# Performance work log

Measured on AMD Instinct MI355X. Metric: run time of the kernel, lower is better.

The kernel has to match this reference:

```python
import jax, jax.numpy as jnp
import numpy as np
from jax import lax

H, W = 320, 320
K = 21
P = (K - 1) // 2  # 10, replicate padding
LAM = 128.0
SIGMA_SPACE = 32.0
SIGMA_LUMA = 8.0
# all (i, j) kernel positions except the center -> 440 offsets
OFFSETS = np.array([(i, j) for i in range(K) for j in range(K)
                    if not (i == P and j == P)], dtype=np.int32)  # [440, 2]


def neighbor_diffs(x):
    """Shift-and-subtract equivalent of the sparse 21x21 conv.

    x: [H, W] -> [440, H, W] where out[k] = x - shift(x, offset_k)
    (replicate padding, matching Conv2d padding_mode='replicate' with a
    +1-at-center / -1-at-(i,j) kernel).
    """
    padded = jnp.pad(x, P, mode='edge')  # [H+2P, W+2P]

    def window(off):
        return lax.dynamic_slice(padded, (off[0], off[1]), (H, W))

    shifted = jax.vmap(window)(jnp.asarray(OFFSETS))  # [440, H, W]
    return x[None, :, :] - shifted


def setup_inputs() -> dict:
    key = jax.random.key(0)
    k_ref, k_tgt, k_noise = jax.random.split(key, 3)
    # random guidance image in [0, 255] like an RGB reference
    reference = jax.random.uniform(k_ref, (H, W, 3), dtype=jnp.float32) * 255.0
    target = jax.random.uniform(k_tgt, (H, W), dtype=jnp.float32)  # target/255
    # output parameter initialized at target (plus tiny noise so the data
    # term is non-degenerate)
    output = target + 0.01 * jax.random.normal(k_noise, (H, W), dtype=jnp.float32)

    # bilateral affinity weights w_ij, exactly as in __init__
    pos_x = jnp.broadcast_to(jnp.linspace(0.0, W, W)[None, :], (H, W))
    pos_y = jnp.broadcast_to(jnp.linspace(0.0, H, H)[:, None], (H, W))
    dpx = neighbor_diffs(pos_x)
    dpy = neighbor_diffs(pos_y)
    position_ij = -(dpx ** 2 + dpy ** 2) / (2.0 * SIGMA_SPACE ** 2)
    reference_ij = 0.0
    for c in range(3):
        reference_ij = reference_ij - neighbor_diffs(reference[:, :, c]) ** 2 / (2.0 * SIGMA_LUMA ** 2)
    w_ij = jnp.exp(position_ij + reference_ij)  # [440, H, W]

    return {"output": output, "target": target, "w_ij": w_ij}


def reference(output, target, w_ij):
    d = neighbor_diffs(output)  # [440, H, W]
    smooth = jnp.mean(w_ij * d * d)
    data = jnp.mean((output - target) ** 2)
    return H * W * LAM * smooth + data
```

## Files before the change

### kernel.cpp

```cpp
#include <hip/hip_runtime.h>
#include <cstddef>

constexpr int H_ = 320;
constexpr int W_ = 320;
constexpr int HW_ = H_ * W_;
constexpr int NK = 440;
constexpr int TS = 32;
constexpr int TPR = W_ / TS;
constexpr int NTILES = TPR * TPR;
constexpr int KC = 20;
constexpr int NKC = NK / KC;
constexpr int SMOOTH_BLOCKS = NTILES * NKC;
constexpr int NPART = SMOOTH_BLOCKS + NTILES;
constexpr int HALO = 10;
constexpr int LW = TS + 2 * HALO;
constexpr int LSTRIDE = LW + 1;

typedef float f32x4 __attribute__((ext_vector_type(4)));

__device__ __forceinline__ int clampi(int v, int lo, int hi) {
    return v < lo ? lo : (v > hi ? hi : v);
}

__device__ __forceinline__ float block_reduce(float v, float* rbuf, int tid) {
    __syncthreads();
    for (int off = 32; off > 0; off >>= 1)
        v += __shfl_down(v, off, 64);
    if ((tid & 63) == 0) rbuf[tid >> 6] = v;
    __syncthreads();
    return rbuf[0] + rbuf[1] + rbuf[2] + rbuf[3];
}

__global__ __launch_bounds__(256) void bsl_main_kernel(
    const float* __restrict__ img,
    const float* __restrict__ tgt,
    const float* __restrict__ w,
    float* __restrict__ partials)
{
    __shared__ float lds[LW * LSTRIDE];
    __shared__ float rbuf[4];
    const int tid = threadIdx.x;

    const int tileId = blockIdx.x / NKC;
    const int kc     = blockIdx.x % NKC;
    const int ty = tileId / TPR, tx = tileId % TPR;
    const int y0 = ty * TS, x0 = tx * TS;

    for (int e = tid; e < LW * LW; e += 256) {
        const int ly = e / LW, lx = e - ly * LW;
        const int gy = clampi(y0 - HALO + ly, 0, H_ - 1);
        const int gx = clampi(x0 - HALO + lx, 0, W_ - 1);
        lds[ly * LSTRIDE + lx] = img[gy * W_ + gx];
    }
    __syncthreads();

    const int row = tid >> 3;
    const int c4  = (tid & 7) * 4;
    const int cbase = (HALO + row) * LSTRIDE + HALO + c4;
    const float c0 = lds[cbase + 0];
    const float c1 = lds[cbase + 1];
    const float c2 = lds[cbase + 2];
    const float c3 = lds[cbase + 3];

    float sacc = 0.f;
    const float* wp = w + (size_t)(kc * KC) * HW_ + (y0 + row) * W_ + x0 + c4;
#pragma unroll 4
    for (int kk = 0; kk < KC; ++kk) {
        const int bk  = kc * KC + kk;
        const int idx = (bk < 220) ? bk : bk + 1;
        const int q   = idx / 21;
        const int di  = q - 10;
        const int dj  = idx - q * 21 - 10;

        const f32x4 w4 = __builtin_nontemporal_load((const f32x4*)wp);
        wp += HW_;

        const int nb = cbase + di * LSTRIDE + dj;
        const float n0 = lds[nb + 0];
        const float n1 = lds[nb + 1];
        const float n2 = lds[nb + 2];
        const float n3 = lds[nb + 3];
        const float d0 = c0 - n0, d1 = c1 - n1, d2 = c2 - n2, d3 = c3 - n3;
        sacc += w4.x * d0 * d0;
        sacc += w4.y * d1 * d1;
        sacc += w4.z * d2 * d2;
        sacc += w4.w * d3 * d3;
    }

    const float ssum = block_reduce(sacc, rbuf, tid);
    if (tid == 0) partials[blockIdx.x] = ssum;

    if (kc == 0) {
        const float4 t4 = *reinterpret_cast<const float4*>(
            tgt + (y0 + row) * W_ + x0 + c4);
        const float d0 = c0 - t4.x, d1 = c1 - t4.y;
        const float d2 = c2 - t4.z, d3 = c3 - t4.w;
        const float dsum = block_reduce(d0*d0 + d1*d1 + d2*d2 + d3*d3, rbuf, tid);
        if (tid == 0) partials[SMOOTH_BLOCKS + tileId] = dsum;
    }
}

__global__ __launch_bounds__(256) void bsl_final_kernel(
    const float* __restrict__ partials, float* __restrict__ out)
{
    const int tid = threadIdx.x;
    double s = 0.0, d = 0.0;

    for (int base = 0; base < SMOOTH_BLOCKS; base += 1024) {
        const int i = base + tid * 4;
        if (i + 4 <= SMOOTH_BLOCKS) {
            const float4 v = *reinterpret_cast<const float4*>(partials + i);
            s += (double)v.x + (double)v.y + (double)v.z + (double)v.w;
        }
    }
    if (tid < NTILES / 4) {
        const float4 v = *reinterpret_cast<const float4*>(
            partials + SMOOTH_BLOCKS + tid * 4);
        d += (double)v.x + (double)v.y + (double)v.z + (double)v.w;
    }

    __shared__ double sm[256];
    __shared__ double sd[256];
    sm[tid] = s; sd[tid] = d;
    __syncthreads();
    for (int st = 128; st > 0; st >>= 1) {
        if (tid < st) { sm[tid] += sm[tid + st]; sd[tid] += sd[tid + st]; }
        __syncthreads();
    }
    if (tid == 0) {
        out[0] = (float)(128.0 * sm[0] / 440.0 + sd[0] / (double)HW_);
    }
}

extern "C" void kernel_launch(void* const* d_in, const int* in_sizes, int n_in,
                              void* d_out, int out_size, void* d_ws, size_t ws_size,
                              hipStream_t stream) {
    const float* img = (const float*)d_in[0];
    const float* tgt = (const float*)d_in[1];
    const float* wij = (const float*)d_in[2];
    float* out = (float*)d_out;
    float* partials = (float*)d_ws;

    bsl_main_kernel<<<SMOOTH_BLOCKS, 256, 0, stream>>>(img, tgt, wij, partials);
    bsl_final_kernel<<<1, 256, 0, stream>>>(partials, out);
}
```

Baseline: 36.26 us.

## Switch to full-width row strips with two rows per thread

Tiles change from 32x32 squares to full-width 8-row strips with 10 offsets per block and 320 threads. Each thread now handles 8 pixels across two rows, so every wij load covers 1280 contiguous floats per warp row and the LDS halo overhead per block shrinks. The trade-off is a larger LDS footprint per block (28x341 floats), a different block count, and a 5-wave reduction.

New measurement: 38.43 us. 6.0% more time.

```diff
diff --git a/kernel.cpp b/kernel.cpp
--- a/kernel.cpp
+++ b/kernel.cpp
@@ -5,16 +5,17 @@
 constexpr int W_ = 320;
 constexpr int HW_ = H_ * W_;
 constexpr int NK = 440;
-constexpr int TS = 32;
-constexpr int TPR = W_ / TS;
-constexpr int NTILES = TPR * TPR;
-constexpr int KC = 20;
+constexpr int TR = 8;
+constexpr int NTILES = H_ / TR;
+constexpr int KC = 10;
 constexpr int NKC = NK / KC;
 constexpr int SMOOTH_BLOCKS = NTILES * NKC;
 constexpr int NPART = SMOOTH_BLOCKS + NTILES;
 constexpr int HALO = 10;
-constexpr int LW = TS + 2 * HALO;
-constexpr int LSTRIDE = LW + 1;
+constexpr int LROWS = TR + 2 * HALO;
+constexpr int LCOLS = W_ + 2 * HALO;
+constexpr int LSTRIDE = LCOLS + 1;
+constexpr int NT_ = 320;
 
 typedef float f32x4 __attribute__((ext_vector_type(4)));
 
@@ -28,74 +29,94 @@
         v += __shfl_down(v, off, 64);
     if ((tid & 63) == 0) rbuf[tid >> 6] = v;
     __syncthreads();
-    return rbuf[0] + rbuf[1] + rbuf[2] + rbuf[3];
+    return rbuf[0] + rbuf[1] + rbuf[2] + rbuf[3] + rbuf[4];
 }
 
-__global__ __launch_bounds__(256) void bsl_main_kernel(
+__global__ __launch_bounds__(NT_, 5) void bsl_main_kernel(
     const float* __restrict__ img,
     const float* __restrict__ tgt,
     const float* __restrict__ w,
     float* __restrict__ partials)
 {
-    __shared__ float lds[LW * LSTRIDE];
-    __shared__ float rbuf[4];
+    __shared__ float lds[LROWS * LSTRIDE];
+    __shared__ float rbuf[5];
     const int tid = threadIdx.x;
 
     const int tileId = blockIdx.x / NKC;
     const int kc     = blockIdx.x % NKC;
-    const int ty = tileId / TPR, tx = tileId % TPR;
-    const int y0 = ty * TS, x0 = tx * TS;
+    const int y0 = tileId * TR;
 
-    for (int e = tid; e < LW * LW; e += 256) {
-        const int ly = e / LW, lx = e - ly * LW;
+    for (int e = tid; e < LROWS * LCOLS; e += NT_) {
+        const int ly = e / LCOLS, lx = e - ly * LCOLS;
         const int gy = clampi(y0 - HALO + ly, 0, H_ - 1);
-        const int gx = clampi(x0 - HALO + lx, 0, W_ - 1);
+        const int gx = clampi(lx - HALO, 0, W_ - 1);
         lds[ly * LSTRIDE + lx] = img[gy * W_ + gx];
     }
     __syncthreads();
 
-    const int row = tid >> 3;
-    const int c4  = (tid & 7) * 4;
-    const int cbase = (HALO + row) * LSTRIDE + HALO + c4;
-    const float c0 = lds[cbase + 0];
-    const float c1 = lds[cbase + 1];
-    const float c2 = lds[cbase + 2];
-    const float c3 = lds[cbase + 3];
+    const int px0 = 4 * tid;
+    const int r0  = px0 / W_;
+    const int cc  = px0 - r0 * W_;
+    const int cb0 = (HALO + r0) * LSTRIDE + HALO + cc;
+    const int cb1 = cb0 + 4 * LSTRIDE;
+    float ca[4], cb[4];
+#pragma unroll
+    for (int j = 0; j < 4; ++j) { ca[j] = lds[cb0 + j]; cb[j] = lds[cb1 + j]; }
 
     float sacc = 0.f;
-    const float* wp = w + (size_t)(kc * KC) * HW_ + (y0 + row) * W_ + x0 + c4;
-#pragma unroll 4
-    for (int kk = 0; kk < KC; ++kk) {
-        const int bk  = kc * KC + kk;
-        const int idx = (bk < 220) ? bk : bk + 1;
-        const int q   = idx / 21;
-        const int di  = q - 10;
-        const int dj  = idx - q * 21 - 10;
+    const float* wq = w + (size_t)(kc * KC) * HW_ + y0 * W_ + px0;
+    for (int kk = 0; kk < KC; kk += 2) {
+        const int bka  = kc * KC + kk;
+        const int idxa = (bka < 220) ? bka : bka + 1;
+        const int qa   = idxa / 21;
+        const int sofa = (qa - 10) * LSTRIDE + (idxa - qa * 21 - 10);
+        const int bkb  = bka + 1;
+        const int idxb = (bkb < 220) ? bkb : bkb + 1;
+        const int qb   = idxb / 21;
+        const int sofb = (qb - 10) * LSTRIDE + (idxb - qb * 21 - 10);
 
-        const f32x4 w4 = __builtin_nontemporal_load((const f32x4*)wp);
-        wp += HW_;
+        const f32x4 wa0 = __builtin_nontemporal_load((const f32x4*)(wq));
+        const f32x4 wa1 = __builtin_nontemporal_load((const f32x4*)(wq + 1280));
+        const f32x4 wb0 = __builtin_nontemporal_load((const f32x4*)(wq + HW_));
+        const f32x4 wb1 = __builtin_nontemporal_load((const f32x4*)(wq + HW_ + 1280));
+        wq += 2 * HW_;
 
-        const int nb = cbase + di * LSTRIDE + dj;
-        const float n0 = lds[nb + 0];
-        const float n1 = lds[nb + 1];
-        const float n2 = lds[nb + 2];
-        const float n3 = lds[nb + 3];
-        const float d0 = c0 - n0, d1 = c1 - n1, d2 = c2 - n2, d3 = c3 - n3;
-        sacc += w4.x * d0 * d0;
-        sacc += w4.y * d1 * d1;
-        sacc += w4.z * d2 * d2;
-        sacc += w4.w * d3 * d3;
+        {
+            const int n0 = cb0 + sofa, n1 = cb1 + sofa;
+            const float d0 = ca[0] - lds[n0 + 0], d1 = ca[1] - lds[n0 + 1];
+            const float d2 = ca[2] - lds[n0 + 2], d3 = ca[3] - lds[n0 + 3];
+            const float e0 = cb[0] - lds[n1 + 0], e1 = cb[1] - lds[n1 + 1];
+            const float e2 = cb[2] - lds[n1 + 2], e3 = cb[3] - lds[n1 + 3];
+            sacc += wa0.x * d0 * d0 + wa0.y * d1 * d1
+                  + wa0.z * d2 * d2 + wa0.w * d3 * d3;
+            sacc += wa1.x * e0 * e0 + wa1.y * e1 * e1
+                  + wa1.z * e2 * e2 + wa1.w * e3 * e3;
+        }
+        {
+            const int n0 = cb0 + sofb, n1 = cb1 + sofb;
+            const float d0 = ca[0] - lds[n0 + 0], d1 = ca[1] - lds[n0 + 1];
+            const float d2 = ca[2] - lds[n0 + 2], d3 = ca[3] - lds[n0 + 3];
+            const float e0 = cb[0] - lds[n1 + 0], e1 = cb[1] - lds[n1 + 1];
+            const float e2 = cb[2] - lds[n1 + 2], e3 = cb[3] - lds[n1 + 3];
+            sacc += wb0.x * d0 * d0 + wb0.y * d1 * d1
+                  + wb0.z * d2 * d2 + wb0.w * d3 * d3;
+            sacc += wb1.x * e0 * e0 + wb1.y * e1 * e1
+                  + wb1.z * e2 * e2 + wb1.w * e3 * e3;
+        }
     }
 
     const float ssum = block_reduce(sacc, rbuf, tid);
     if (tid == 0) partials[blockIdx.x] = ssum;
 
     if (kc == 0) {
-        const float4 t4 = *reinterpret_cast<const float4*>(
-            tgt + (y0 + row) * W_ + x0 + c4);
-        const float d0 = c0 - t4.x, d1 = c1 - t4.y;
-        const float d2 = c2 - t4.z, d3 = c3 - t4.w;
-        const float dsum = block_reduce(d0*d0 + d1*d1 + d2*d2 + d3*d3, rbuf, tid);
+        const float4 t0 = *reinterpret_cast<const float4*>(tgt + y0 * W_ + px0);
+        const float4 t1 = *reinterpret_cast<const float4*>(tgt + y0 * W_ + 1280 + px0);
+        const float d0 = ca[0] - t0.x, d1 = ca[1] - t0.y;
+        const float d2 = ca[2] - t0.z, d3 = ca[3] - t0.w;
+        const float e0 = cb[0] - t1.x, e1 = cb[1] - t1.y;
+        const float e2 = cb[2] - t1.z, e3 = cb[3] - t1.w;
+        const float dsum = block_reduce(d0*d0 + d1*d1 + d2*d2 + d3*d3
+                                      + e0*e0 + e1*e1 + e2*e2 + e3*e3, rbuf, tid);
         if (tid == 0) partials[SMOOTH_BLOCKS + tileId] = dsum;
     }
 }
@@ -141,6 +162,6 @@
     float* out = (float*)d_out;
     float* partials = (float*)d_ws;
 
-    bsl_main_kernel<<<SMOOTH_BLOCKS, 256, 0, stream>>>(img, tgt, wij, partials);
+    bsl_main_kernel<<<SMOOTH_BLOCKS, NT_, 0, stream>>>(img, tgt, wij, partials);
     bsl_final_kernel<<<1, 256, 0, stream>>>(partials, out);
 }
```

## Distribute tile-offset work evenly over fixed 2048 blocks with software prefetch

Applied to the files above, without the earlier changes.

Replaces the fixed tile×offset-chunk grid (2200 blocks of 20 offsets) with 2048 blocks that each take a contiguous, evenly split range of the 44,000 (tile, offset) work items, reloading the tile halo into LDS whenever a range crosses into a new tile. It also double-buffers the nontemporal weight loads two iterations ahead and splits the accumulator into two chains. The aim is to balance work across CUs and keep more weight loads in flight on this memory-bound kernel. In exchange, blocks whose range spans a tile boundary pay an extra LDS refill and barrier, and the data-term reduction now runs inside the loop.

Result: slower. 42.85 us (+18.2%).

```diff
diff --git a/kernel.cpp b/kernel.cpp
--- a/kernel.cpp
+++ b/kernel.cpp
@@ -8,10 +8,9 @@
 constexpr int TS = 32;
 constexpr int TPR = W_ / TS;
 constexpr int NTILES = TPR * TPR;
-constexpr int KC = 20;
-constexpr int NKC = NK / KC;
-constexpr int SMOOTH_BLOCKS = NTILES * NKC;
-constexpr int NPART = SMOOTH_BLOCKS + NTILES;
+constexpr int NWORK = NTILES * NK;
+constexpr int NB = 2048;
+constexpr int NPART = NB + NTILES;
 constexpr int HALO = 10;
 constexpr int LW = TS + 2 * HALO;
 constexpr int LSTRIDE = LW + 1;
@@ -40,64 +39,76 @@
     __shared__ float lds[LW * LSTRIDE];
     __shared__ float rbuf[4];
     const int tid = threadIdx.x;
+    const int b = blockIdx.x;
 
-    const int tileId = blockIdx.x / NKC;
-    const int kc     = blockIdx.x % NKC;
-    const int ty = tileId / TPR, tx = tileId % TPR;
-    const int y0 = ty * TS, x0 = tx * TS;
-
-    for (int e = tid; e < LW * LW; e += 256) {
-        const int ly = e / LW, lx = e - ly * LW;
-        const int gy = clampi(y0 - HALO + ly, 0, H_ - 1);
-        const int gx = clampi(x0 - HALO + lx, 0, W_ - 1);
-        lds[ly * LSTRIDE + lx] = img[gy * W_ + gx];
-    }
-    __syncthreads();
+    const int r0 = (int)(((long long)b * NWORK) >> 11);
+    const int r1 = (int)(((long long)(b + 1) * NWORK) >> 11);
 
     const int row = tid >> 3;
     const int c4  = (tid & 7) * 4;
-    const int cbase = (HALO + row) * LSTRIDE + HALO + c4;
-    const float c0 = lds[cbase + 0];
-    const float c1 = lds[cbase + 1];
-    const float c2 = lds[cbase + 2];
-    const float c3 = lds[cbase + 3];
 
-    float sacc = 0.f;
-    const float* wp = w + (size_t)(kc * KC) * HW_ + (y0 + row) * W_ + x0 + c4;
-#pragma unroll 4
-    for (int kk = 0; kk < KC; ++kk) {
-        const int bk  = kc * KC + kk;
-        const int idx = (bk < 220) ? bk : bk + 1;
-        const int q   = idx / 21;
-        const int di  = q - 10;
-        const int dj  = idx - q * 21 - 10;
+    float sacc = 0.f, sacc2 = 0.f;
 
-        const f32x4 w4 = __builtin_nontemporal_load((const f32x4*)wp);
-        wp += HW_;
+    for (int item = r0; item < r1; ) {
+        const int t  = item / NK;
+        const int ks = item - t * NK;
+        const int span = r1 - item;
+        const int ke = (NK - ks < span) ? NK : ks + span;
+        const int y0 = (t / TPR) * TS, x0 = (t % TPR) * TS;
 
-        const int nb = cbase + di * LSTRIDE + dj;
-        const float n0 = lds[nb + 0];
-        const float n1 = lds[nb + 1];
-        const float n2 = lds[nb + 2];
-        const float n3 = lds[nb + 3];
-        const float d0 = c0 - n0, d1 = c1 - n1, d2 = c2 - n2, d3 = c3 - n3;
-        sacc += w4.x * d0 * d0;
-        sacc += w4.y * d1 * d1;
-        sacc += w4.z * d2 * d2;
-        sacc += w4.w * d3 * d3;
+        if (item != r0) __syncthreads();
+        for (int e = tid; e < LW * LW; e += 256) {
+            const int ly = e / LW, lx = e - ly * LW;
+            const int gy = clampi(y0 - HALO + ly, 0, H_ - 1);
+            const int gx = clampi(x0 - HALO + lx, 0, W_ - 1);
+            lds[ly * LSTRIDE + lx] = img[gy * W_ + gx];
+        }
+        __syncthreads();
+
+        const int cbase = (HALO + row) * LSTRIDE + HALO + c4;
+        const float c0 = lds[cbase + 0];
+        const float c1 = lds[cbase + 1];
+        const float c2 = lds[cbase + 2];
+        const float c3 = lds[cbase + 3];
+
+        const float* wp = w + (size_t)ks * HW_ + (y0 + row) * W_ + x0 + c4;
+        f32x4 wv0 = __builtin_nontemporal_load((const f32x4*)wp);
+        f32x4 wv1 = (ks + 1 < ke)
+            ? __builtin_nontemporal_load((const f32x4*)(wp + HW_)) : wv0;
+
+        for (int kk = ks; kk < ke; ++kk) {
+            const f32x4 wnext = (kk + 2 < ke)
+                ? __builtin_nontemporal_load((const f32x4*)(wp + 2 * HW_)) : wv1;
+
+            const int idx = (kk < 220) ? kk : kk + 1;
+            const int q   = idx / 21;
+            const int nb  = cbase + (q - 10) * LSTRIDE + (idx - q * 21 - 10);
+
+            const float d0 = c0 - lds[nb + 0];
+            const float d1 = c1 - lds[nb + 1];
+            const float d2 = c2 - lds[nb + 2];
+            const float d3 = c3 - lds[nb + 3];
+            sacc  += wv0.x * d0 * d0 + wv0.y * d1 * d1;
+            sacc2 += wv0.z * d2 * d2 + wv0.w * d3 * d3;
+
+            wv0 = wv1; wv1 = wnext; wp += HW_;
+        }
+
+        if (ks == 0) {
+            const float4 t4 = *reinterpret_cast<const float4*>(
+                tgt + (y0 + row) * W_ + x0 + c4);
+            const float d0 = c0 - t4.x, d1 = c1 - t4.y;
+            const float d2 = c2 - t4.z, d3 = c3 - t4.w;
+            const float dsum = block_reduce(d0*d0 + d1*d1 + d2*d2 + d3*d3,
+                                            rbuf, tid);
+            if (tid == 0) partials[NB + t] = dsum;
+        }
+
+        item += ke - ks;
     }
 
-    const float ssum = block_reduce(sacc, rbuf, tid);
-    if (tid == 0) partials[blockIdx.x] = ssum;
-
-    if (kc == 0) {
-        const float4 t4 = *reinterpret_cast<const float4*>(
-            tgt + (y0 + row) * W_ + x0 + c4);
-        const float d0 = c0 - t4.x, d1 = c1 - t4.y;
-        const float d2 = c2 - t4.z, d3 = c3 - t4.w;
-        const float dsum = block_reduce(d0*d0 + d1*d1 + d2*d2 + d3*d3, rbuf, tid);
-        if (tid == 0) partials[SMOOTH_BLOCKS + tileId] = dsum;
-    }
+    const float ssum = block_reduce(sacc + sacc2, rbuf, tid);
+    if (tid == 0) partials[b] = ssum;
 }
 
 __global__ __launch_bounds__(256) void bsl_final_kernel(
@@ -106,16 +117,12 @@
     const int tid = threadIdx.x;
     double s = 0.0, d = 0.0;
 
-    for (int base = 0; base < SMOOTH_BLOCKS; base += 1024) {
-        const int i = base + tid * 4;
-        if (i + 4 <= SMOOTH_BLOCKS) {
-            const float4 v = *reinterpret_cast<const float4*>(partials + i);
-            s += (double)v.x + (double)v.y + (double)v.z + (double)v.w;
-        }
+    for (int base = 0; base < NB; base += 1024) {
+        const float4 v = *reinterpret_cast<const float4*>(partials + base + tid * 4);
+        s += (double)v.x + (double)v.y + (double)v.z + (double)v.w;
     }
     if (tid < NTILES / 4) {
-        const float4 v = *reinterpret_cast<const float4*>(
-            partials + SMOOTH_BLOCKS + tid * 4);
+        const float4 v = *reinterpret_cast<const float4*>(partials + NB + tid * 4);
         d += (double)v.x + (double)v.y + (double)v.z + (double)v.w;
     }
 
@@ -141,6 +148,6 @@
     float* out = (float*)d_out;
     float* partials = (float*)d_ws;
 
-    bsl_main_kernel<<<SMOOTH_BLOCKS, 256, 0, stream>>>(img, tgt, wij, partials);
+    bsl_main_kernel<<<NB, 256, 0, stream>>>(img, tgt, wij, partials);
     bsl_final_kernel<<<1, 256, 0, stream>>>(partials, out);
 }
```
